# Optimization experiments

Measured on AMD Instinct MI355X. Metric: run time of the kernel, lower is better.

Reference implementation:

```python
import jax, jax.numpy as jnp
import numpy as np

B, N, C_IN, C_COORD, K = 2, 8192, 64, 3, 16
C_CAT = C_IN + C_COORD  # 67
HID1, HID2, C_OUT = 32, 64, 64


def setup_inputs() -> dict:
    key = jax.random.key(0)
    ks = jax.random.split(key, 10)
    s = 0.05
    return {
        "point_features": jax.random.normal(ks[0], (B, N, C_IN), jnp.float32),
        "coords": jax.random.uniform(ks[1], (B, N, C_COORD), jnp.float32),
        "w1": jax.random.normal(ks[2], (HID1, C_CAT), jnp.float32) * s,
        "b1": jax.random.normal(ks[3], (HID1,), jnp.float32) * s,
        "w2": jax.random.normal(ks[4], (HID2, HID1), jnp.float32) * s,
        "b2": jax.random.normal(ks[5], (HID2,), jnp.float32) * s,
        "w3": jax.random.normal(ks[6], (C_OUT, HID2), jnp.float32) * s,
        "b3": jax.random.normal(ks[7], (C_OUT,), jnp.float32) * s,
        "aggr_w": jax.random.normal(ks[8], (K,), jnp.float32) * s,
        "aggr_b": jax.random.normal(ks[9], (1,), jnp.float32) * s,
    }


def _knn_idx(coords):
    # squared pairwise distances: [B, N, N]
    sq = jnp.sum(coords * coords, axis=-1)
    d2 = sq[:, :, None] + sq[:, None, :] - 2.0 * jnp.einsum("bnc,bmc->bnm", coords, coords)
    # k smallest distances -> top_k of negated; self (d=0) lands at slot 0
    _, idx = jax.lax.top_k(-d2, K)  # [B, N, K]
    return idx


def reference(point_features, coords, w1, b1, w2, b2, w3, b3, aggr_w, aggr_b):
    idx = _knn_idx(coords)  # [B, N, K] int32
    feats = jnp.concatenate([point_features, coords], axis=-1)  # [B, N, C_CAT]
    # gather neighbor features -> [B, N, K, C_CAT]
    g = jax.vmap(lambda f, i: f[i])(feats, idx)
    # relative coords w.r.t. neighbor 0 (self)
    rel = g[..., -C_COORD:] - g[:, :, 0:1, -C_COORD:]
    g = jnp.concatenate([g[..., :C_IN], rel], axis=-1)
    # point pooling: max over K of raw input-feature channels
    y_pool = jnp.max(g[..., :C_IN], axis=2)  # [B, N, C_IN]
    # kernel MLP: stacked 1x1 convs, NO activations (act_func=None in source)
    h = jnp.einsum("bnkc,oc->bnko", g, w1) + b1
    h = jnp.einsum("bnkc,oc->bnko", h, w2) + b2
    h = jnp.einsum("bnkc,oc->bnko", h, w3) + b3  # [B, N, K, C_OUT]
    # attentive aggregation: Conv2d(K, 1, 1) over the K axis
    y_aggr = jnp.einsum("bnko,k->bno", h, aggr_w) + aggr_b  # [B, N, C_OUT]
    out_sum = jnp.sum(h, axis=2)  # [B, N, C_OUT]
    # concat order matches torch: (sum, pool, aggr), then permute -> B x N x C'
    return jnp.concatenate([out_sum, y_pool, y_aggr], axis=-1)
```

## Files before the change

### kernel.cpp

```cpp
#include <hip/hip_runtime.h>
#include <stdint.h>


typedef unsigned short u16;
typedef unsigned int   u32;
typedef unsigned long long u64;

#define NPTS  8192
#define KNB   16
#define SCAP  128
#define CAPA  512
#define QPW   8

__device__ __forceinline__ float bf2f(u16 u) {
    union { u32 i; float f; } v; v.i = ((u32)u) << 16; return v.f;
}
__device__ __forceinline__ u16 f2bf(float f) {
    u32 x = __float_as_uint(f);
    return (u16)((x + 0x7FFFu + ((x >> 16) & 1u)) >> 16);
}
__device__ __forceinline__ u32 fordkey(float f) {
    u32 u = __float_as_uint(f);
    return u ^ ((u32)((int)u >> 31) | 0x80000000u);
}
__device__ __forceinline__ u64 shflxor64(u64 v, int m) {
    int lo = __shfl_xor((int)(u32)v, m, 64);
    int hi = __shfl_xor((int)(u32)(v >> 32), m, 64);
    return ((u64)(u32)hi << 32) | (u32)lo;
}
__device__ __forceinline__ void wave_fence() {
    asm volatile("s_waitcnt lgkmcnt(0)" ::: "memory");
    __builtin_amdgcn_sched_barrier(0);
}
__device__ __forceinline__ float sq_np32(float x, float y, float z) {
    return __fadd_rn(__fadd_rn(__fmul_rn(x, x), __fmul_rn(y, y)), __fmul_rn(z, z));
}
__device__ __forceinline__ float d2_ref(float qx, float qy, float qz, float qsq,
                                        float x, float y, float z, float sq) {
    float dot = fmaf(z, qz, fmaf(y, qy, __fmul_rn(x, qx)));
    return __fsub_rn(__fadd_rn(qsq, sq), __fmul_rn(2.0f, dot));
}
__device__ __forceinline__ int cellof(float v) {
    int c = (int)floorf(v * 8.0f);
    return c < 0 ? 0 : (c > 7 ? 7 : c);
}

__global__ __launch_bounds__(256) void pack_count_kernel(
    const float* __restrict__ pf, const float* __restrict__ coords,
    u16* __restrict__ pfh, int* __restrict__ counts) {
    int gid = blockIdx.x * 256 + threadIdx.x;
    pfh[gid] = f2bf(pf[gid]);
    if (gid < 2 * NPTS) {
        float x = coords[gid * 3 + 0];
        float y = coords[gid * 3 + 1];
        float z = coords[gid * 3 + 2];
        int b = gid >> 13;
        int cell = (cellof(x) * 8 + cellof(y)) * 8 + cellof(z);
        atomicAdd(&counts[b * 512 + cell], 1);
    }
}

__global__ __launch_bounds__(512) void scan_kernel(
    const int* __restrict__ counts, int* __restrict__ cellStart,
    int* __restrict__ cellOffset) {
    __shared__ int s[512];
    int b = blockIdx.x, t = threadIdx.x;
    int myc = counts[b * 512 + t];
    s[t] = myc; __syncthreads();
#pragma unroll
    for (int off = 1; off < 512; off <<= 1) {
        int v = (t >= off) ? s[t - off] : 0; __syncthreads();
        s[t] += v; __syncthreads();
    }
    int excl = s[t] - myc;
    cellStart[b * 513 + t] = excl;
    cellOffset[b * 512 + t] = excl;
    if (t == 511) cellStart[b * 513 + 512] = s[511];
}

__global__ __launch_bounds__(256) void scatter_kernel(
    const float* __restrict__ coords, int* __restrict__ cellOffset,
    float4* __restrict__ spts, int* __restrict__ sidx) {
    int gid = blockIdx.x * 256 + threadIdx.x;
    float x = coords[gid * 3 + 0];
    float y = coords[gid * 3 + 1];
    float z = coords[gid * 3 + 2];
    int b = gid >> 13, i = gid & (NPTS - 1);
    int cell = (cellof(x) * 8 + cellof(y)) * 8 + cellof(z);
    int pos = atomicAdd(&cellOffset[b * 512 + cell], 1);
    spts[b * NPTS + pos] = make_float4(x, y, z, sq_np32(x, y, z));
    sidx[b * NPTS + pos] = i;
}

__device__ __forceinline__ void scan_seg(
    const float4* __restrict__ sp, const int* __restrict__ cs,
    u64* __restrict__ surv, int base, int z0, int z1,
    float qx, float qy, float qz, float qsq, float tau, int lane, int& cnt) {
    if (z0 > z1) return;
    int s = cs[base + z0], e = cs[base + z1 + 1];
    for (int i0 = s; i0 < e; i0 += 64) {
        int i = i0 + lane;
        bool valid = (i < e);
        int ii = valid ? i : (e - 1);
        float4 c = sp[ii];
        float d2 = d2_ref(qx, qy, qz, qsq, c.x, c.y, c.z, c.w);
        bool pass = valid && (d2 <= tau);
        u64 mask = __ballot(pass);
        if (pass) {
            int pre = __builtin_amdgcn_mbcnt_hi((u32)(mask >> 32),
                      __builtin_amdgcn_mbcnt_lo((u32)mask, 0));
            int pos = cnt + pre;
            if (pos < SCAP)
                surv[pos] = ((u64)fordkey(d2) << 32) | (u32)ii;
        }
        cnt += (int)__popcll(mask);
    }
}

__global__ __launch_bounds__(256, 6) void knn_kernel(
    const float4* __restrict__ spts, const int* __restrict__ sidx,
    const int* __restrict__ cellStart, int* __restrict__ idx_out) {
    __shared__ u64 allk_s[4][CAPA];
    __shared__ u64 surv_s[4][SCAP];

    const int lane = threadIdx.x & 63;
    const int wid  = threadIdx.x >> 6;
    u64* __restrict__ allk = allk_s[wid];
    u64* __restrict__ surv = surv_s[wid];

    const int blk  = blockIdx.x;
    const int sblk = (blk & 7) * 512 + (blk >> 3);
    const int p    = sblk * 4 + wid;
    const int b    = p >> 13;
    const float4* sp = spts + b * NPTS;
    const int*    si = sidx + b * NPTS;
    const int*    cs = cellStart + b * 513;

    float4 qc = sp[p & (NPTS - 1)];
    const float qx = qc.x, qy = qc.y, qz = qc.z, qsq = qc.w;
    int cqx = cellof(qx), cqy = cellof(qy), cqz = cellof(qz);

    const int ucqx = __builtin_amdgcn_readfirstlane(cqx);
    const int ucqy = __builtin_amdgcn_readfirstlane(cqy);
    const int ucqz = __builtin_amdgcn_readfirstlane(cqz);

    const int ax0 = max(ucqx - 1, 0), ax1 = min(ucqx + 1, 7);
    const int ay0 = max(ucqy - 1, 0), ay1 = min(ucqy + 1, 7);
    const int az0 = max(ucqz - 1, 0), az1 = min(ucqz + 1, 7);

    int segS[9], segE[9];
#pragma unroll
    for (int u = 0; u < 9; ++u) {
        int cx = ucqx - 1 + (u / 3);
        int cy = ucqy - 1 + (u % 3);
        bool ok = (cx >= 0) && (cx <= 7) && (cy >= 0) && (cy <= 7);
        if (ok) {
            int base = (cx * 8 + cy) * 8;
            segS[u] = cs[base + az0];
            segE[u] = cs[base + az1 + 1];
        } else {
            segS[u] = 0;
            segE[u] = 0;
        }
    }

    float dmin = 3.0e38f;
    int cnt0 = 0;
    bool ovf = false;
#pragma unroll
    for (int u = 0; u < 9; ++u) {
        int s = segS[u], e = segE[u];
#pragma unroll 1
        for (int i0 = s; i0 < e; i0 += 64) {
            int i = i0 + lane;
            bool valid = (i < e);
            int ii = valid ? i : (e - 1);
            float4 c = sp[ii];
            float d2 = d2_ref(qx, qy, qz, qsq, c.x, c.y, c.z, c.w);
            if (valid) dmin = fminf(dmin, d2);
            int add = (e - i0 < 64) ? (e - i0) : 64;
            if (!ovf && cnt0 + add <= CAPA) {
                if (valid)
                    allk[cnt0 + lane] = ((u64)fordkey(d2) << 32) | (u32)ii;
                cnt0 += add;
            } else {
                ovf = true;
            }
        }
    }
    wave_fence();

    {
        float v = dmin;
#pragma unroll
        for (int k = 2; k <= 64; k <<= 1) {
#pragma unroll
            for (int j2 = k >> 1; j2 >= 1; j2 >>= 1) {
                float o = __shfl_xor(v, j2, 64);
                bool lo = (lane & j2) == 0;
                bool up = (lane & k) == 0;
                float mn = fminf(v, o), mx = fmaxf(v, o);
                v = (lo == up) ? mn : mx;
            }
        }
        dmin = __shfl(v, 15, 64);
    }
    const float tau = dmin;

    float rr = sqrtf(tau + 1e-5f) + 1e-6f;
    int bx0 = max((int)floorf((qx - rr) * 8.0f), 0);
    int bx1 = min((int)floorf((qx + rr) * 8.0f), 7);
    int by0 = max((int)floorf((qy - rr) * 8.0f), 0);
    int by1 = min((int)floorf((qy + rr) * 8.0f), 7);
    int bz0 = max((int)floorf((qz - rr) * 8.0f), 0);
    int bz1 = min((int)floorf((qz + rr) * 8.0f), 7);
    int cnt = 0;
    if (!ovf) {
        const u32 taukey = fordkey(tau);
        for (int i0 = 0; i0 < cnt0; i0 += 64) {
            int i = i0 + lane;
            bool valid = (i < cnt0);
            u64 kk = valid ? allk[i] : ~0ull;
            bool pass = valid && ((u32)(kk >> 32) <= taukey);
            u64 mask = __ballot(pass);
            if (pass) {
                int pre = __builtin_amdgcn_mbcnt_hi((u32)(mask >> 32),
                          __builtin_amdgcn_mbcnt_lo((u32)mask, 0));
                int pos = cnt + pre;
                if (pos < SCAP) surv[pos] = kk;
            }
            cnt += (int)__popcll(mask);
        }
    }
#pragma unroll 1
    for (int cx = bx0; cx <= bx1; ++cx)
#pragma unroll 1
        for (int cy = by0; cy <= by1; ++cy) {
            int base = (cx * 8 + cy) * 8;
            bool colInA = !ovf && cx >= ax0 && cx <= ax1 &&
                          cy >= ay0 && cy <= ay1;
            if (colInA) {
                scan_seg(sp, cs, surv, base, bz0, min(az0 - 1, bz1),
                         qx, qy, qz, qsq, tau, lane, cnt);
                scan_seg(sp, cs, surv, base, max(az1 + 1, bz0), bz1,
                         qx, qy, qz, qsq, tau, lane, cnt);
            } else {
                scan_seg(sp, cs, surv, base, bz0, bz1,
                         qx, qy, qz, qsq, tau, lane, cnt);
            }
        }
    wave_fence();

    int myidx = 0;
    if (cnt <= 64) {
        u32 k32 = 0xffffffffu, p32 = 0xffffffffu;
        if (lane < cnt) {
            u64 kk = surv[lane];
            k32 = (u32)(kk >> 32);
            p32 = (u32)kk;
        }
#pragma unroll
        for (int k = 2; k <= 64; k <<= 1) {
#pragma unroll
            for (int j2 = k >> 1; j2 >= 1; j2 >>= 1) {
                u32 ok = (u32)__shfl_xor((int)k32, j2, 64);
                u32 op = (u32)__shfl_xor((int)p32, j2, 64);
                bool lo = (lane & j2) == 0;
                bool up = (lane & k) == 0;
                bool takemin = (lo == up);
                bool less = (ok < k32) || (ok == k32 && op < p32);
                bool take = (less == takemin);
                k32 = take ? ok : k32;
                p32 = take ? op : p32;
            }
        }
        myidx = (int)p32;
    } else {
        int cc = cnt > SCAP ? SCAP : cnt;
        u64 a0 = (lane < cc) ? surv[lane] : ~0ull;
        u64 a1 = (64 + lane < cc) ? surv[64 + lane] : ~0ull;
        if (a1 < a0) { u64 tmp = a0; a0 = a1; a1 = tmp; }
#pragma unroll 1
        for (int r = 0; r < 16; ++r) {
            u64 m = a0;
#pragma unroll
            for (int d = 1; d < 64; d <<= 1) {
                u64 o = shflxor64(m, d);
                m = (o < m) ? o : m;
            }
            if (a0 == m) { a0 = a1; a1 = ~0ull; }
            if (lane == r) myidx = (int)(u32)(m & 0xffffffffu);
        }
    }
    if (lane < KNB) {
        const int q = si[p & (NPTS - 1)];
        idx_out[((size_t)b * NPTS + q) * KNB + lane] =
            si[myidx & (NPTS - 1)];
    }
}

__global__ __launch_bounds__(64) void mlp_kernel(
    const u16* __restrict__ pfh, const float* __restrict__ coords,
    const float* __restrict__ w1, const float* __restrict__ b1,
    const float* __restrict__ w2, const float* __restrict__ b2,
    const float* __restrict__ w3, const float* __restrict__ b3,
    const float* __restrict__ aw, const float* __restrict__ ab,
    const int* __restrict__ knn_idx, const int* __restrict__ sidx,
    float* __restrict__ out) {

    __shared__ __attribute__((aligned(16))) float wstage[4160];
    __shared__ __attribute__((aligned(16))) float vbuf[2][68];
    __shared__ __attribute__((aligned(16))) float h1buf[2][36];

    const int lane = threadIdx.x;
    const int r    = lane & 31;
    const int vec  = lane >> 5;

#pragma unroll
    for (int i0 = 0; i0 < 2144; i0 += 64) {
        int i = i0 + lane;
        if (i < 2144) {
            int row = i / 67;
            int col = i - row * 67;
            wstage[row * 69 + col] = w1[i];
        }
    }
    wave_fence();
    float w1r[68];
#pragma unroll
    for (int c = 0; c < 67; ++c) w1r[c] = wstage[r * 69 + c];
    w1r[67] = 0.0f;
    wave_fence();

#pragma unroll
    for (int i0 = 0; i0 < 2048; i0 += 64) {
        int i = i0 + lane;
        wstage[(i >> 5) * 33 + (i & 31)] = w2[i];
    }
    wave_fence();
    float w2r[32];
#pragma unroll
    for (int c = 0; c < 32; ++c) w2r[c] = wstage[lane * 33 + c];
    wave_fence();

#pragma unroll
    for (int i0 = 0; i0 < 4096; i0 += 64) {
        int i = i0 + lane;
        wstage[(i >> 6) * 65 + (i & 63)] = w3[i];
    }
    wave_fence();
    float w3r[64];
#pragma unroll
    for (int c = 0; c < 64; ++c) w3r[c] = wstage[lane * 65 + c];

    float awr[16];
#pragma unroll
    for (int k = 0; k < 16; ++k) awr[k] = aw[k];
    float sa = 0.0f;
#pragma unroll
    for (int k = 0; k < 16; ++k) sa += awr[k];
    const float b1v = b1[r], b2v = b2[lane], b3v = b3[lane], abv = ab[0];
    const float c1 = (vec == 0) ? 16.0f : sa;

    const int sblk = (blockIdx.x & 7) * 256 + (blockIdx.x >> 3);

#pragma unroll 1
    for (int t = 0; t < QPW; ++t) {
        const int gp = sblk * QPW + t;
        const int b  = gp >> 13;
        const int q  = sidx[(size_t)b * NPTS + (gp & (NPTS - 1))];
        const int gq = b * NPTS + q;
        const u16*   pfb = pfh + (size_t)b * NPTS * 64;
        const float* cb  = coords + (size_t)b * NPTS * 3;

        int myi = knn_idx[(size_t)gq * KNB + (lane & 15)] & (NPTS - 1);

        float pool = -3.0e38f, G1 = 0.0f, Ga = 0.0f;
#pragma unroll
        for (int k = 0; k < 16; ++k) {
            int nk = __shfl(myi, k, 64);
            float v = bf2f(pfb[nk * 64 + lane]);
            pool = fmaxf(pool, v);
            G1 += v;
            Ga = fmaf(awr[k], v, Ga);
        }
        vbuf[0][lane] = G1;
        vbuf[1][lane] = Ga;

        if (lane < 48) {
            int j  = lane >> 4;
            int i0 = __shfl(myi, 0, 64);
            float rel  = cb[myi * 3 + j] - cb[i0 * 3 + j];
            float wrel = awr[lane & 15] * rel;
#pragma unroll
            for (int d = 1; d < 16; d <<= 1) {
                rel  += __shfl_xor(rel, d, 64);
                wrel += __shfl_xor(wrel, d, 64);
            }
            if ((lane & 15) == 0) { vbuf[0][64 + j] = rel; vbuf[1][64 + j] = wrel; }
        }
        if (lane == 0) { vbuf[0][67] = 0.0f; vbuf[1][67] = 0.0f; }
        __syncthreads();

        float acc = c1 * b1v;
        {
            const float4* vp = (const float4*)(&vbuf[vec][0]);
#pragma unroll
            for (int c4 = 0; c4 < 17; ++c4) {
                float4 g4 = vp[c4];
                acc = fmaf(g4.x, w1r[c4 * 4 + 0], acc);
                acc = fmaf(g4.y, w1r[c4 * 4 + 1], acc);
                acc = fmaf(g4.z, w1r[c4 * 4 + 2], acc);
                acc = fmaf(g4.w, w1r[c4 * 4 + 3], acc);
            }
        }
        h1buf[vec][r] = acc;
        __syncthreads();

        float a0 = 16.0f * b2v, a1 = sa * b2v;
        {
            const float4* p0 = (const float4*)(&h1buf[0][0]);
            const float4* p1 = (const float4*)(&h1buf[1][0]);
#pragma unroll
            for (int c4 = 0; c4 < 8; ++c4) {
                float4 x0 = p0[c4], x1 = p1[c4];
                a0 = fmaf(x0.x, w2r[c4 * 4 + 0], a0);
                a0 = fmaf(x0.y, w2r[c4 * 4 + 1], a0);
                a0 = fmaf(x0.z, w2r[c4 * 4 + 2], a0);
                a0 = fmaf(x0.w, w2r[c4 * 4 + 3], a0);
                a1 = fmaf(x1.x, w2r[c4 * 4 + 0], a1);
                a1 = fmaf(x1.y, w2r[c4 * 4 + 1], a1);
                a1 = fmaf(x1.z, w2r[c4 * 4 + 2], a1);
                a1 = fmaf(x1.w, w2r[c4 * 4 + 3], a1);
            }
        }
        __syncthreads();
        vbuf[0][lane] = a0;
        vbuf[1][lane] = a1;
        __syncthreads();

        float s1 = 16.0f * b3v, sA = sa * b3v;
        {
            const float4* p0 = (const float4*)(&vbuf[0][0]);
            const float4* p1 = (const float4*)(&vbuf[1][0]);
#pragma unroll
            for (int c4 = 0; c4 < 16; ++c4) {
                float4 x0 = p0[c4], x1 = p1[c4];
                s1 = fmaf(x0.x, w3r[c4 * 4 + 0], s1);
                s1 = fmaf(x0.y, w3r[c4 * 4 + 1], s1);
                s1 = fmaf(x0.z, w3r[c4 * 4 + 2], s1);
                s1 = fmaf(x0.w, w3r[c4 * 4 + 3], s1);
                sA = fmaf(x1.x, w3r[c4 * 4 + 0], sA);
                sA = fmaf(x1.y, w3r[c4 * 4 + 1], sA);
                sA = fmaf(x1.z, w3r[c4 * 4 + 2], sA);
                sA = fmaf(x1.w, w3r[c4 * 4 + 3], sA);
            }
        }
        float* op = out + (size_t)gq * 192;
        op[lane]       = s1;
        op[64 + lane]  = pool;
        op[128 + lane] = sA + abv;
        __syncthreads();
    }
}

extern "C" void kernel_launch(void* const* d_in, const int* in_sizes, int n_in,
                              void* d_out, int out_size, void* d_ws, size_t ws_size,
                              hipStream_t stream) {
    const float* pf     = (const float*)d_in[0];
    const float* coords = (const float*)d_in[1];
    const float* w1     = (const float*)d_in[2];
    const float* b1     = (const float*)d_in[3];
    const float* w2     = (const float*)d_in[4];
    const float* b2     = (const float*)d_in[5];
    const float* w3     = (const float*)d_in[6];
    const float* b3     = (const float*)d_in[7];
    const float* aw     = (const float*)d_in[8];
    const float* ab     = (const float*)d_in[9];

    char* ws = (char*)d_ws;
    int*    knn_idx    = (int*)ws;
    u16*    pfh        = (u16*)(ws + (1 << 20));
    float4* spts       = (float4*)(ws + (3 << 20));
    int*    sidx       = (int*)(ws + (3 << 20) + (256 << 10));
    int*    cellStart  = (int*)(ws + (3 << 20) + (320 << 10));
    int*    counts     = (int*)(ws + (3 << 20) + (328 << 10));
    int*    cellOffset = (int*)(ws + (3 << 20) + (336 << 10));
    float*  outp       = (float*)d_out;

    hipMemsetAsync(counts, 0, 2 * 512 * sizeof(int), stream);
    pack_count_kernel<<<4096, 256, 0, stream>>>(pf, coords, pfh, counts);
    scan_kernel<<<2, 512, 0, stream>>>(counts, cellStart, cellOffset);
    scatter_kernel<<<64, 256, 0, stream>>>(coords, cellOffset, spts, sidx);
    knn_kernel<<<4096, 256, 0, stream>>>(spts, sidx, cellStart, knn_idx);
    mlp_kernel<<<2048, 64, 0, stream>>>(pfh, coords, w1, b1, w2, b2, w3, b3,
                                        aw, ab, knn_idx, sidx, outp);
}
```

Baseline: 143.1 us.

## Run four waves per MLP block sharing LDS weights, read w3 from LDS

The MLP kernel now launches 256-thread blocks of four waves instead of single-wave blocks. All three weight matrices are staged once per block in shared memory, and each wave handles 4 query points with its own private scratch buffers. Block barriers inside the loop become wave-level fences, and w3 is read from LDS instead of being held in 64 registers, which cuts register pressure and allows more waves per CU. In exchange, every w3 access becomes an LDS load, and each point's work is spread across more waves with fewer points per wave.

```diff
diff --git a/kernel.cpp b/kernel.cpp
--- a/kernel.cpp
+++ b/kernel.cpp
@@ -10,7 +10,6 @@
 #define KNB   16
 #define SCAP  128
 #define CAPA  512
-#define QPW   8
 
 __device__ __forceinline__ float bf2f(u16 u) {
     union { u32 i; float f; } v; v.i = ((u32)u) << 16; return v.f;
@@ -299,7 +298,7 @@
     }
 }
 
-__global__ __launch_bounds__(64) void mlp_kernel(
+__global__ __launch_bounds__(256, 4) void mlp_kernel(
     const u16* __restrict__ pfh, const float* __restrict__ coords,
     const float* __restrict__ w1, const float* __restrict__ b1,
     const float* __restrict__ w2, const float* __restrict__ b2,
@@ -308,50 +307,48 @@
     const int* __restrict__ knn_idx, const int* __restrict__ sidx,
     float* __restrict__ out) {
 
-    __shared__ __attribute__((aligned(16))) float wstage[4160];
-    __shared__ __attribute__((aligned(16))) float vbuf[2][68];
-    __shared__ __attribute__((aligned(16))) float h1buf[2][36];
-
-    const int lane = threadIdx.x;
+    __shared__ __attribute__((aligned(16))) float w1s[2208];
+    __shared__ __attribute__((aligned(16))) float w2s[2112];
+    __shared__ __attribute__((aligned(16))) float w3s[4160];
+    __shared__ __attribute__((aligned(16))) float vbuf_s[4][2][68];
+    __shared__ __attribute__((aligned(16))) float h1buf_s[4][2][36];
+
+    const int tid  = threadIdx.x;
+    const int lane = tid & 63;
+    const int wid  = tid >> 6;
     const int r    = lane & 31;
     const int vec  = lane >> 5;
-
-#pragma unroll
-    for (int i0 = 0; i0 < 2144; i0 += 64) {
-        int i = i0 + lane;
+    float (*vbuf)[68]  = vbuf_s[wid];
+    float (*h1buf)[36] = h1buf_s[wid];
+
+#pragma unroll
+    for (int i0 = 0; i0 < 2144; i0 += 256) {
+        int i = i0 + tid;
         if (i < 2144) {
             int row = i / 67;
             int col = i - row * 67;
-            wstage[row * 69 + col] = w1[i];
-        }
-    }
-    wave_fence();
+            w1s[row * 69 + col] = w1[i];
+        }
+    }
+#pragma unroll
+    for (int i0 = 0; i0 < 2048; i0 += 256) {
+        int i = i0 + tid;
+        w2s[(i >> 5) * 33 + (i & 31)] = w2[i];
+    }
+#pragma unroll
+    for (int i0 = 0; i0 < 4096; i0 += 256) {
+        int i = i0 + tid;
+        w3s[(i >> 6) * 65 + (i & 63)] = w3[i];
+    }
+    __syncthreads();
+
     float w1r[68];
 #pragma unroll
-    for (int c = 0; c < 67; ++c) w1r[c] = wstage[r * 69 + c];
+    for (int c = 0; c < 67; ++c) w1r[c] = w1s[r * 69 + c];
     w1r[67] = 0.0f;
-    wave_fence();
-
-#pragma unroll
-    for (int i0 = 0; i0 < 2048; i0 += 64) {
-        int i = i0 + lane;
-        wstage[(i >> 5) * 33 + (i & 31)] = w2[i];
-    }
-    wave_fence();
     float w2r[32];
 #pragma unroll
-    for (int c = 0; c < 32; ++c) w2r[c] = wstage[lane * 33 + c];
-    wave_fence();
-
-#pragma unroll
-    for (int i0 = 0; i0 < 4096; i0 += 64) {
-        int i = i0 + lane;
-        wstage[(i >> 6) * 65 + (i & 63)] = w3[i];
-    }
-    wave_fence();
-    float w3r[64];
-#pragma unroll
-    for (int c = 0; c < 64; ++c) w3r[c] = wstage[lane * 65 + c];
+    for (int c = 0; c < 32; ++c) w2r[c] = w2s[lane * 33 + c];
 
     float awr[16];
 #pragma unroll
@@ -362,11 +359,12 @@
     const float b1v = b1[r], b2v = b2[lane], b3v = b3[lane], abv = ab[0];
     const float c1 = (vec == 0) ? 16.0f : sa;
 
-    const int sblk = (blockIdx.x & 7) * 256 + (blockIdx.x >> 3);
+    const int sblk = (blockIdx.x & 7) * 128 + (blockIdx.x >> 3);
+    const int gp0  = sblk * 16 + wid * 4;
 
 #pragma unroll 1
-    for (int t = 0; t < QPW; ++t) {
-        const int gp = sblk * QPW + t;
+    for (int t = 0; t < 4; ++t) {
+        const int gp = gp0 + t;
         const int b  = gp >> 13;
         const int q  = sidx[(size_t)b * NPTS + (gp & (NPTS - 1))];
         const int gq = b * NPTS + q;
@@ -400,7 +398,7 @@
             if ((lane & 15) == 0) { vbuf[0][64 + j] = rel; vbuf[1][64 + j] = wrel; }
         }
         if (lane == 0) { vbuf[0][67] = 0.0f; vbuf[1][67] = 0.0f; }
-        __syncthreads();
+        wave_fence();
 
         float acc = c1 * b1v;
         {
@@ -415,7 +413,7 @@
             }
         }
         h1buf[vec][r] = acc;
-        __syncthreads();
+        wave_fence();
 
         float a0 = 16.0f * b2v, a1 = sa * b2v;
         {
@@ -434,33 +432,38 @@
                 a1 = fmaf(x1.w, w2r[c4 * 4 + 3], a1);
             }
         }
-        __syncthreads();
+        wave_fence();
         vbuf[0][lane] = a0;
         vbuf[1][lane] = a1;
-        __syncthreads();
+        wave_fence();
 
         float s1 = 16.0f * b3v, sA = sa * b3v;
         {
             const float4* p0 = (const float4*)(&vbuf[0][0]);
             const float4* p1 = (const float4*)(&vbuf[1][0]);
+            const float*  w3row = &w3s[lane * 65];
 #pragma unroll
             for (int c4 = 0; c4 < 16; ++c4) {
                 float4 x0 = p0[c4], x1 = p1[c4];
-                s1 = fmaf(x0.x, w3r[c4 * 4 + 0], s1);
-                s1 = fmaf(x0.y, w3r[c4 * 4 + 1], s1);
-                s1 = fmaf(x0.z, w3r[c4 * 4 + 2], s1);
-                s1 = fmaf(x0.w, w3r[c4 * 4 + 3], s1);
-                sA = fmaf(x1.x, w3r[c4 * 4 + 0], sA);
-                sA = fmaf(x1.y, w3r[c4 * 4 + 1], sA);
-                sA = fmaf(x1.z, w3r[c4 * 4 + 2], sA);
-                sA = fmaf(x1.w, w3r[c4 * 4 + 3], sA);
+                float wa = w3row[c4 * 4 + 0];
+                float wb = w3row[c4 * 4 + 1];
+                float wc = w3row[c4 * 4 + 2];
+                float wd = w3row[c4 * 4 + 3];
+                s1 = fmaf(x0.x, wa, s1);
+                s1 = fmaf(x0.y, wb, s1);
+                s1 = fmaf(x0.z, wc, s1);
+                s1 = fmaf(x0.w, wd, s1);
+                sA = fmaf(x1.x, wa, sA);
+                sA = fmaf(x1.y, wb, sA);
+                sA = fmaf(x1.z, wc, sA);
+                sA = fmaf(x1.w, wd, sA);
             }
         }
         float* op = out + (size_t)gq * 192;
         op[lane]       = s1;
         op[64 + lane]  = pool;
         op[128 + lane] = sA + abv;
-        __syncthreads();
+        wave_fence();
     }
 }
 
@@ -493,6 +496,6 @@
     scan_kernel<<<2, 512, 0, stream>>>(counts, cellStart, cellOffset);
     scatter_kernel<<<64, 256, 0, stream>>>(coords, cellOffset, spts, sidx);
     knn_kernel<<<4096, 256, 0, stream>>>(spts, sidx, cellStart, knn_idx);
-    mlp_kernel<<<2048, 64, 0, stream>>>(pfh, coords, w1, b1, w2, b2, w3, b3,
-                                        aw, ab, knn_idx, sidx, outp);
-}
+    mlp_kernel<<<1024, 256, 0, stream>>>(pfh, coords, w1, b1, w2, b2, w3, b3,
+                                         aw, ab, knn_idx, sidx, outp);
+}
```

New measurement: 172.3 us. 20.4% more time.
